# Optimization experiments

Measured on AMD Instinct MI355X. Metric: run time of the kernel, lower is better.

Reference implementation:

```python
import jax, jax.numpy as jnp
import numpy as np

D_MODEL = 1024
N_HEADS = 16
HEAD_DIM = D_MODEL // N_HEADS  # 64
WINDOW = 128
LOCAL_BLOCK = 256
LATENT_TOKENS = 64
LATENT_D = 256
LATENT_HEADS = 4
LATENT_HD = LATENT_D // LATENT_HEADS  # 64
NEG = -1e9


def setup_inputs() -> dict:
    key = jax.random.key(0)
    ks = jax.random.split(key, 14)
    B, S = 2, 4096
    s = 0.02
    f32 = jnp.float32
    return {
        "x": jax.random.normal(ks[0], (B, S, D_MODEL), f32),
        "qkv_w": jax.random.normal(ks[1], (D_MODEL, 3 * D_MODEL), f32) * s,
        "qkv_b": jnp.zeros((3 * D_MODEL,), f32),
        "rq_w": jax.random.normal(ks[2], (D_MODEL, LATENT_D), f32) * s,
        "rq_b": jnp.zeros((LATENT_D,), f32),
        "rkv_w": jax.random.normal(ks[3], (D_MODEL, 2 * LATENT_D), f32) * s,
        "rkv_b": jnp.zeros((2 * LATENT_D,), f32),
        "rout_w": jax.random.normal(ks[4], (LATENT_D, D_MODEL), f32) * s,
        "rout_b": jnp.zeros((D_MODEL,), f32),
        "out_w": jax.random.normal(ks[5], (D_MODEL, D_MODEL), f32) * s,
        "out_b": jnp.zeros((D_MODEL,), f32),
        "gl_w": jax.random.normal(ks[6], (HEAD_DIM, 1), f32) * s,
        "gr_w": jax.random.normal(ks[7], (HEAD_DIM, 1), f32) * s,
    }


def _local_attention(q, k, v):
    # q,k,v: [B,H,S,hd]. Blockwise causal local attention: query i attends to
    # keys at distance d with 0 < d <= WINDOW (strictly past, self excluded).
    B, H, S, hd = q.shape
    bs = min(S, max(WINDOW, LOCAL_BLOCK))
    nb = S // bs  # S chosen divisible by bs
    w = WINDOW
    L = bs + w - 1  # key span per query block
    k_pad = jnp.pad(k, ((0, 0), (0, 0), (w - 1, 0), (0, 0)))
    v_pad = jnp.pad(v, ((0, 0), (0, 0), (w - 1, 0), (0, 0)))
    starts = jnp.arange(nb) * bs
    idx = starts[:, None] + jnp.arange(L)[None, :]  # [nb,L] into padded axis
    kb = k_pad[:, :, idx]  # [B,H,nb,L,hd]
    vb = v_pad[:, :, idx]
    qb = q.reshape(B, H, nb, bs, hd)
    q_pos = starts[:, None] + jnp.arange(bs)[None, :]            # [nb,bs]
    k_gpos = starts[:, None] + jnp.arange(L)[None, :] - (w - 1)   # [nb,L]
    dist = q_pos[:, :, None] - k_gpos[:, None, :]                 # [nb,bs,L]
    allowed = (dist > 0) & (dist <= w) & (k_gpos[:, None, :] >= 0)
    scale = 1.0 / np.sqrt(hd)
    scores = jnp.einsum('bhnqd,bhnkd->bhnqk', qb, kb) * scale
    scores = jnp.where(allowed, scores, NEG)
    attn = jax.nn.softmax(scores, axis=-1)
    # query 0 has no valid keys (self excluded) -> output 0 for that row
    attn = jnp.where(allowed.any(-1)[None, None, :, :, None], attn, 0.0)
    out = jnp.einsum('bhnqk,bhnkd->bhnqd', attn, vb)
    return out.reshape(B, H, S, hd)


def reference(x, qkv_w, qkv_b, rq_w, rq_b, rkv_w, rkv_b, rout_w, rout_b,
              out_w, out_b, gl_w, gr_w):
    B, S, D = x.shape
    # ---- local branch ----
    qkv = x @ qkv_w + qkv_b  # [B,S,3D]
    q, k, v = jnp.split(qkv, 3, axis=-1)
    def heads(t):
        return t.reshape(B, S, N_HEADS, HEAD_DIM).transpose(0, 2, 1, 3)
    local = _local_attention(heads(q), heads(k), heads(v))  # [B,H,S,hd]
    # ---- pooled latents ----
    chunk = -(-S // min(LATENT_TOKENS, S))  # ceil; S divisible here
    nlat = S // chunk
    pooled = x.reshape(B, nlat, chunk, D).mean(axis=2)  # [B,L,D]
    chunk_ids = jnp.arange(S) // chunk                   # [S]
    # ---- latent cross-attention ----
    rq = (x @ rq_w + rq_b).reshape(B, S, LATENT_HEADS, LATENT_HD).transpose(0, 2, 1, 3)
    rkv = pooled @ rkv_w + rkv_b
    rk, rv = jnp.split(rkv, 2, axis=-1)
    rk = rk.reshape(B, nlat, LATENT_HEADS, LATENT_HD).transpose(0, 2, 1, 3)
    rv = rv.reshape(B, nlat, LATENT_HEADS, LATENT_HD).transpose(0, 2, 1, 3)
    lscale = 1.0 / np.sqrt(LATENT_HD)
    lscores = jnp.einsum('bhsd,bhld->bhsl', rq, rk) * lscale  # [B,Hl,S,L]
    lat_allowed = jnp.arange(nlat)[None, :] < chunk_ids[:, None]  # strictly past chunks
    lscores = jnp.where(lat_allowed[None, None], lscores, NEG)
    lattn = jax.nn.softmax(lscores, axis=-1)
    lattn = jnp.where(lat_allowed.any(-1)[None, None, :, None], lattn, 0.0)
    lat_out = jnp.einsum('bhsl,bhld->bhsd', lattn, rv)  # [B,Hl,S,hdl]
    lat_out = lat_out.transpose(0, 2, 1, 3).reshape(B, S, LATENT_D)
    remote = (lat_out @ rout_w + rout_b)                 # [B,S,D]
    remote_h = remote.reshape(B, S, N_HEADS, HEAD_DIM).transpose(0, 2, 1, 3)
    # ---- learned per-head gate mixing local/remote ----
    gate = jax.nn.sigmoid(local @ gl_w + remote_h @ gr_w)  # [B,H,S,1]
    mixed = gate * local + (1.0 - gate) * remote_h
    mixed = mixed.transpose(0, 2, 1, 3).reshape(B, S, D)
    return mixed @ out_w + out_b
```

## Files before the change

### kernel.cpp

```cpp
#include <hip/hip_runtime.h>

typedef __bf16 bf16;
typedef bf16 bf16x4 __attribute__((ext_vector_type(4)));
typedef bf16 bf16x8 __attribute__((ext_vector_type(8)));
typedef float f32x4 __attribute__((ext_vector_type(4)));

#define B_ 2
#define S_ 4096
#define D_ 1024
#define QSTR 3328

__device__ __forceinline__ void gload_lds16(const void* g, void* l) {
  __builtin_amdgcn_global_load_lds((const __attribute__((address_space(1))) void*)g,
                                   (__attribute__((address_space(3))) void*)l, 16, 0, 0);
}

__device__ __forceinline__ void transpose_block(
    const float* __restrict__ in, bf16* __restrict__ out, int K, int N,
    int bx, int by, float (*tile)[33], int tx, int ty)
{
  const int nb = bx * 32, kb = by * 32;
#pragma unroll
  for (int j = 0; j < 4; j++)
    tile[ty + j * 8][tx] = in[(size_t)(kb + ty + j * 8) * N + nb + tx];
  __syncthreads();
#pragma unroll
  for (int j = 0; j < 4; j++)
    out[(size_t)(nb + ty + j * 8) * K + kb + tx] = (bf16)tile[tx][ty + j * 8];
}

__global__ __launch_bounds__(256) void prep_kernel(
    const float* __restrict__ qkv_w, const float* __restrict__ rq_w,
    const float* __restrict__ rkv_w, const float* __restrict__ rout_w,
    const float* __restrict__ out_w, const float* __restrict__ x,
    const float* __restrict__ qkv_b, const float* __restrict__ rq_b,
    bf16* __restrict__ qkvr_wt, bf16* __restrict__ rkv_wt,
    bf16* __restrict__ rout_wt, bf16* __restrict__ out_wt,
    bf16* __restrict__ xb, float* __restrict__ qkvr_b)
{
  __shared__ float tile[32][33];
  const int t = threadIdx.x;
  const int tx = t & 31, ty = t >> 5;
  int bid = blockIdx.x;
  if (bid < 3072) {
    transpose_block(qkv_w, qkvr_wt, 1024, 3072, bid % 96, bid / 96, tile, tx, ty);
    return;
  }
  bid -= 3072;
  if (bid < 256) {
    transpose_block(rq_w, qkvr_wt + (size_t)3072 * 1024, 1024, 256, bid % 8, bid / 8, tile, tx, ty);
    return;
  }
  bid -= 256;
  if (bid < 512) {
    transpose_block(rkv_w, rkv_wt, 1024, 512, bid % 16, bid / 16, tile, tx, ty);
    return;
  }
  bid -= 512;
  if (bid < 256) {
    transpose_block(rout_w, rout_wt, 256, 1024, bid % 32, bid / 32, tile, tx, ty);
    return;
  }
  bid -= 256;
  if (bid < 1024) {
    transpose_block(out_w, out_wt, 1024, 1024, bid % 32, bid / 32, tile, tx, ty);
    return;
  }
  bid -= 1024;
  if (bid < 2048) {
    const int n4 = B_ * S_ * 1024 / 4;
    for (int i = bid * 256 + t; i < n4; i += 2048 * 256) {
      const float4 v = ((const float4*)x)[i];
      bf16x4 o = {(bf16)v.x, (bf16)v.y, (bf16)v.z, (bf16)v.w};
      *(bf16x4*)&xb[i * 4] = o;
    }
    return;
  }
  {
    for (int i = t; i < 3072; i += 256) qkvr_b[i] = qkv_b[i];
    if (t < 256) qkvr_b[3072 + t] = rq_b[t];
  }
}

template <typename OutT>
__global__ __launch_bounds__(256) void gemm_bias_kernel(
    const bf16* __restrict__ A, const bf16* __restrict__ Bt,
    const float* __restrict__ bias, OutT* __restrict__ C,
    int M, int N, int K)
{
  __shared__ __align__(16) bf16 Al[128 * 32];
  __shared__ __align__(16) bf16 Bl[128 * 32];
  const int m0 = blockIdx.x * 128;
  const int n0 = blockIdx.y * 128;
  const int t = threadIdx.x;
  const int lane = t & 63;
  const int wave = t >> 6;
  const int wr = (wave >> 1) * 64;
  const int wc = (wave & 1) * 64;
  const int r16 = lane & 15;
  const int kg = lane >> 4;

  f32x4 acc[4][4];
#pragma unroll
  for (int i = 0; i < 4; i++)
#pragma unroll
    for (int j = 0; j < 4; j++) {
      f32x4 z = {0.f, 0.f, 0.f, 0.f};
      acc[i][j] = z;
    }

  for (int k0 = 0; k0 < K; k0 += 32) {
    __syncthreads();
#pragma unroll
    for (int i = 0; i < 2; i++) {
      const int o = i * 4096 + wave * 1024 + lane * 16;
      const int r = o >> 6;
      const int cb = o & 63;
      gload_lds16((const char*)(A + (size_t)(m0 + r) * K + k0) + cb,
                  (char*)Al + i * 4096 + wave * 1024);
      gload_lds16((const char*)(Bt + (size_t)(n0 + r) * K + k0) + cb,
                  (char*)Bl + i * 4096 + wave * 1024);
    }
    __syncthreads();
    bf16x8 a[4], b[4];
#pragma unroll
    for (int i = 0; i < 4; i++)
      a[i] = *(const bf16x8*)&Al[(wr + i * 16 + r16) * 32 + kg * 8];
#pragma unroll
    for (int i = 0; i < 4; i++)
      b[i] = *(const bf16x8*)&Bl[(wc + i * 16 + r16) * 32 + kg * 8];
#pragma unroll
    for (int i = 0; i < 4; i++)
#pragma unroll
      for (int j = 0; j < 4; j++)
        acc[i][j] = __builtin_amdgcn_mfma_f32_16x16x32_bf16(a[i], b[j], acc[i][j], 0, 0, 0);
  }

  float bs[4];
#pragma unroll
  for (int j = 0; j < 4; j++) bs[j] = bias[n0 + wc + j * 16 + r16];
#pragma unroll
  for (int i = 0; i < 4; i++)
#pragma unroll
    for (int j = 0; j < 4; j++)
#pragma unroll
      for (int r = 0; r < 4; r++) {
        const int row = m0 + wr + i * 16 + kg * 4 + r;
        const int col = n0 + wc + j * 16 + r16;
        C[(size_t)row * N + col] = (OutT)(acc[i][j][r] + bs[j]);
      }
}

template <typename OutT>
__global__ __launch_bounds__(512, 1) void gemm8_kernel(
    const bf16* __restrict__ A, const bf16* __restrict__ Bt,
    const float* __restrict__ bias, OutT* __restrict__ C,
    int M, int N, int K)
{
  __shared__ __align__(16) bf16 Al[2][256 * 64];
  __shared__ __align__(16) bf16 Bl[2][256 * 64];

  const int nbx = gridDim.x;
  const int nwg = nbx * gridDim.y;
  int bid = blockIdx.y * nbx + blockIdx.x;
  bid = (bid & 7) * (nwg >> 3) + (bid >> 3);
  const int m0 = (bid % nbx) * 256;
  const int n0 = (bid / nbx) * 256;

  const int t = threadIdx.x;
  const int lane = t & 63;
  const int w = t >> 6;
  const int wm = w >> 2;
  const int wn = w & 3;
  const int l15 = lane & 15;
  const int kg = lane >> 4;

  const int srow = t >> 3;
  const int schunk = (t & 7) ^ (srow & 7);
  const bf16* Aaddr = A + (size_t)(m0 + srow) * K + schunk * 8;
  const bf16* Baddr = Bt + (size_t)(n0 + srow) * K + schunk * 8;

  const int NT = K >> 6;
  const int NITER = NT >> 1;

  const int arow = wm * 128 + l15;
  const int brow = wn * 64 + l15;
  const int c0 = (kg ^ (l15 & 7)) * 16;
  const int c1 = ((4 + kg) ^ (l15 & 7)) * 16;

  f32x4 acc[8][4];
#pragma unroll
  for (int i = 0; i < 8; i++)
#pragma unroll
    for (int j = 0; j < 4; j++) { f32x4 z = {0, 0, 0, 0}; acc[i][j] = z; }

#define STG_A(buf, q, kt) gload_lds16(Aaddr + (size_t)(q) * 64 * K + (kt) * 64, \
                                      (char*)&Al[buf][0] + (q) * 8192 + w * 1024)
#define STG_B(buf, q, kt) gload_lds16(Baddr + (size_t)(q) * 64 * K + (kt) * 64, \
                                      (char*)&Bl[buf][0] + (q) * 8192 + w * 1024)
#define RD_A(buf, aq) \
  _Pragma("unroll") for (int ii = 0; ii < 4; ii++) { \
    const char* p_ = (const char*)&Al[buf][0] + (size_t)(arow + (aq) * 64 + ii * 16) * 128; \
    af[ii][0] = *(const bf16x8*)(p_ + c0); \
    af[ii][1] = *(const bf16x8*)(p_ + c1); }
#define RD_B(buf) \
  _Pragma("unroll") for (int jj = 0; jj < 4; jj++) { \
    const char* p_ = (const char*)&Bl[buf][0] + (size_t)(brow + jj * 16) * 128; \
    bfr[jj][0] = *(const bf16x8*)(p_ + c0); \
    bfr[jj][1] = *(const bf16x8*)(p_ + c1); }
#define MM(iofs, j0) \
  _Pragma("unroll") for (int ii = 0; ii < 4; ii++) \
  _Pragma("unroll") for (int jj = (j0); jj < (j0) + 2; jj++) { \
    acc[(iofs) + ii][jj] = __builtin_amdgcn_mfma_f32_16x16x32_bf16(af[ii][0], bfr[jj][0], acc[(iofs) + ii][jj], 0, 0, 0); \
    acc[(iofs) + ii][jj] = __builtin_amdgcn_mfma_f32_16x16x32_bf16(af[ii][1], bfr[jj][1], acc[(iofs) + ii][jj], 0, 0, 0); }
#define BARX __builtin_amdgcn_s_barrier()
#define LGKM0 do { asm volatile("s_waitcnt lgkmcnt(0)" ::: "memory"); \
                   __builtin_amdgcn_sched_barrier(0); } while (0)
#define PRI1 __builtin_amdgcn_s_setprio(1)
#define PRI0 __builtin_amdgcn_s_setprio(0)

#pragma unroll
  for (int q = 0; q < 4; q++) { STG_B(0, q, 0); }
#pragma unroll
  for (int q = 0; q < 4; q++) { STG_A(0, q, 0); }
#pragma unroll
  for (int q = 0; q < 4; q++) { STG_B(1, q, 1); }
#pragma unroll
  for (int q = 0; q < 4; q++) { STG_A(1, q, 1); }
  asm volatile("s_waitcnt vmcnt(8)" ::: "memory");
  BARX;

  bf16x8 af[4][2], bfr[4][2];

  for (int it = 0; it < NITER; it++) {
    const int kt0 = 2 * it;
    const bool st = (it + 1) < NITER;

    RD_A(0, 0); RD_B(0);
    BARX; LGKM0; PRI1; MM(0, 0); PRI0; BARX;
    if (st) { STG_B(0, 0, kt0 + 2); STG_B(0, 1, kt0 + 2); }
    PRI1; MM(0, 2); PRI0; BARX;
    RD_A(0, 1);
    if (st) { STG_B(0, 2, kt0 + 2); STG_B(0, 3, kt0 + 2); }
    BARX; LGKM0; PRI1; MM(4, 0); PRI0; BARX;
    if (st) { STG_A(0, 0, kt0 + 2); STG_A(0, 2, kt0 + 2); }
    PRI1; MM(4, 2); PRI0;
    asm volatile("s_waitcnt vmcnt(6)" ::: "memory");
    BARX;

    RD_A(1, 0); RD_B(1);
    if (st) { STG_A(0, 1, kt0 + 2); STG_A(0, 3, kt0 + 2); }
    BARX; LGKM0; PRI1; MM(0, 0); PRI0; BARX;
    if (st) { STG_B(1, 0, kt0 + 3); STG_B(1, 1, kt0 + 3); }
    PRI1; MM(0, 2); PRI0; BARX;
    RD_A(1, 1);
    if (st) { STG_B(1, 2, kt0 + 3); STG_B(1, 3, kt0 + 3); }
    BARX; LGKM0; PRI1; MM(4, 0); PRI0; BARX;
    if (st) { STG_A(1, 0, kt0 + 3); STG_A(1, 1, kt0 + 3);
              STG_A(1, 2, kt0 + 3); STG_A(1, 3, kt0 + 3); }
    PRI1; MM(4, 2); PRI0;
    asm volatile("s_waitcnt vmcnt(8)" ::: "memory");
    BARX;
  }

#undef STG_A
#undef STG_B
#undef RD_A
#undef RD_B
#undef MM
#undef BARX
#undef LGKM0
#undef PRI1
#undef PRI0

  float bs[4];
#pragma unroll
  for (int j = 0; j < 4; j++) bs[j] = bias[n0 + wn * 64 + j * 16 + l15];
#pragma unroll
  for (int i = 0; i < 8; i++)
#pragma unroll
    for (int j = 0; j < 4; j++)
#pragma unroll
      for (int rr = 0; rr < 4; rr++) {
        const int row = m0 + wm * 128 + i * 16 + kg * 4 + rr;
        const int col = n0 + wn * 64 + j * 16 + l15;
        C[(size_t)row * N + col] = (OutT)(acc[i][j][rr] + bs[j]);
      }
}

__global__ __launch_bounds__(256) void pool_rkv_kernel(
    const bf16* __restrict__ xb, const bf16* __restrict__ rkv_wt,
    const float* __restrict__ rkv_b, bf16* __restrict__ rkvb)
{
  __shared__ float prow[1024];
  const int blk = blockIdx.x;
  const int b = blk >> 6, lt = blk & 63;
  const int t = threadIdx.x;

  const bf16* px = xb + ((size_t)b * S_ + lt * 64) * 1024 + t * 4;
  float s0 = 0.f, s1 = 0.f, s2 = 0.f, s3 = 0.f;
#pragma unroll
  for (int c = 0; c < 64; c++) {
    bf16x4 v = *(const bf16x4*)(px + (size_t)c * 1024);
    s0 += (float)v[0]; s1 += (float)v[1]; s2 += (float)v[2]; s3 += (float)v[3];
  }
  prow[t * 4 + 0] = s0 * 0.015625f;
  prow[t * 4 + 1] = s1 * 0.015625f;
  prow[t * 4 + 2] = s2 * 0.015625f;
  prow[t * 4 + 3] = s3 * 0.015625f;
  __syncthreads();

  const int n = blockIdx.y * 256 + t;
  const bf16* wcol = rkv_wt + (size_t)n * 1024;
  float s = rkv_b[n];
#pragma unroll 4
  for (int k = 0; k < 1024; k += 8) {
    bf16x8 wv = *(const bf16x8*)(wcol + k);
#pragma unroll
    for (int j = 0; j < 8; j++) s += prow[k + j] * (float)wv[j];
  }
  rkvb[(size_t)blk * 512 + n] = (bf16)s;
}

__global__ __launch_bounds__(256) void latent_attn_kernel(
    const bf16* __restrict__ qkvrb, const bf16* __restrict__ rkvb,
    bf16* __restrict__ latout)
{
  __shared__ float rq_s[256];
  __shared__ float attn_s[4][64];
  const int blk = blockIdx.x;
  const int b = blk >> 12, s = blk & 4095;
  const int t = threadIdx.x;
  const int h = t >> 6, l = t & 63;
  const int cid = s >> 6;
  rq_s[t] = (float)qkvrb[((size_t)b * S_ + s) * QSTR + 3072 + t];
  __syncthreads();
  float val = -1e30f;
  if (l < cid) {
    const bf16* kr = rkvb + (size_t)(b * 64 + l) * 512 + h * 64;
    float sum = 0.f;
#pragma unroll
    for (int c = 0; c < 8; c++) {
      bf16x8 kv = *(const bf16x8*)(kr + c * 8);
#pragma unroll
      for (int j = 0; j < 8; j++) sum += rq_s[h * 64 + c * 8 + j] * (float)kv[j];
    }
    val = sum * 0.125f;
  }
  float mx = val;
#pragma unroll
  for (int off = 32; off; off >>= 1) mx = fmaxf(mx, __shfl_xor(mx, off));
  const float p = (l < cid) ? __expf(val - mx) : 0.f;
  float sm = p;
#pragma unroll
  for (int off = 32; off; off >>= 1) sm += __shfl_xor(sm, off);
  attn_s[h][l] = (sm > 0.f) ? p / sm : 0.f;
  __syncthreads();
  float o = 0.f;
  const bf16* vb = rkvb + (size_t)b * 64 * 512 + 256 + h * 64 + l;
  for (int lat = 0; lat < cid; lat++) o += attn_s[h][lat] * (float)vb[(size_t)lat * 512];
  latout[((size_t)b * S_ + s) * 256 + h * 64 + l] = (bf16)o;
}

__global__ __launch_bounds__(256) void local_attn_gate(
    const bf16* __restrict__ qkv, const bf16* __restrict__ remote,
    const float* __restrict__ glw, const float* __restrict__ grw,
    bf16* __restrict__ mixedb)
{
  __shared__ __align__(16) bf16 Kl[128 * 72];
  __shared__ __align__(16) bf16 Vt[64 * 136];
  __shared__ __align__(16) bf16 Pl[4][16 * 136];

  const int q0 = blockIdx.x * 128;
  const int h  = blockIdx.y;
  const int b  = blockIdx.z;
  const int t  = threadIdx.x;
  const int w  = t >> 6;
  const int l  = t & 63;
  const int g  = l >> 4;
  const int l15 = l & 15;

  const bf16* qbase = qkv + (size_t)b * S_ * QSTR + h * 64;
  const bf16* kbase = qbase + 1024;
  const bf16* vbase = qbase + 2048;

  bf16* PlW = &Pl[w][0];

  const int kq = (t & 31) * 4;
  const int dh = (t >> 5) * 8;

  bf16x8 qf[2][2];
#pragma unroll
  for (int sl = 0; sl < 2; sl++) {
    const int j = sl ? 7 - w : w;
#pragma unroll
    for (int db = 0; db < 2; db++)
      qf[sl][db] = *(const bf16x8*)(qbase + (size_t)(q0 + j * 16 + l15) * QSTR + db * 32 + g * 8);
  }

  float m_[2][4], l_[2][4];
  f32x4 accO[2][4];
#pragma unroll
  for (int sl = 0; sl < 2; sl++) {
#pragma unroll
    for (int r = 0; r < 4; r++) { m_[sl][r] = -1e30f; l_[sl][r] = 0.f; }
#pragma unroll
    for (int dt = 0; dt < 4; dt++) { f32x4 z = {0,0,0,0}; accO[sl][dt] = z; }
  }

  const int tstart = (q0 == 0) ? 1 : 0;

  bf16x8 kreg[4], vreg[4];
  {
    const int base = q0 - 128 + tstart * 128;
#pragma unroll
    for (int i = 0; i < 4; i++) {
      const int c = i * 256 + t;
      const int kk = c >> 3, dc = c & 7;
      kreg[i] = *(const bf16x8*)(kbase + (size_t)(base + kk) * QSTR + dc * 8);
    }
#pragma unroll
    for (int i = 0; i < 4; i++)
      vreg[i] = *(const bf16x8*)(vbase + (size_t)(base + kq + i) * QSTR + dh);
  }

  for (int tile = tstart; tile < 2; tile++) {
    __syncthreads();
#pragma unroll
    for (int i = 0; i < 4; i++) {
      const int c = i * 256 + t;
      const int kk = c >> 3, dc = c & 7;
      *(bf16x8*)&Kl[kk * 72 + dc * 8] = kreg[i];
    }
#pragma unroll
    for (int j = 0; j < 8; j++) {
      bf16x4 wv = {vreg[0][j], vreg[1][j], vreg[2][j], vreg[3][j]};
      *(bf16x4*)&Vt[(dh + j) * 136 + kq] = wv;
    }
    __syncthreads();
    if (tile == 0) {
#pragma unroll
      for (int i = 0; i < 4; i++) {
        const int c = i * 256 + t;
        const int kk = c >> 3, dc = c & 7;
        kreg[i] = *(const bf16x8*)(kbase + (size_t)(q0 + kk) * QSTR + dc * 8);
      }
#pragma unroll
      for (int i = 0; i < 4; i++)
        vreg[i] = *(const bf16x8*)(vbase + (size_t)(q0 + kq + i) * QSTR + dh);
    }

#pragma unroll
    for (int sl = 0; sl < 2; sl++) {
      const int j = sl ? 7 - w : w;
      const int lo = (tile == 0) ? (j & ~1) : 0;
      const int hi = (tile == 0) ? 8 : ((j & ~1) + 2);

      f32x4 s[8];
#pragma unroll
      for (int kk = 0; kk < 8; kk++) {
        if (kk < lo || kk >= hi) continue;
        f32x4 z = {0,0,0,0};
        s[kk] = z;
        const bf16x8 kf0 = *(const bf16x8*)&Kl[(kk * 16 + l15) * 72 + g * 8];
        const bf16x8 kf1 = *(const bf16x8*)&Kl[(kk * 16 + l15) * 72 + 32 + g * 8];
        s[kk] = __builtin_amdgcn_mfma_f32_16x16x32_bf16(qf[sl][0], kf0, s[kk], 0, 0, 0);
        s[kk] = __builtin_amdgcn_mfma_f32_16x16x32_bf16(qf[sl][1], kf1, s[kk], 0, 0, 0);
      }
#pragma unroll
      for (int kk = 0; kk < 8; kk++) {
        if (kk < lo || kk >= hi) continue;
        const int kr = kk * 16 + l15;
#pragma unroll
        for (int r = 0; r < 4; r++) {
          const int qr = j * 16 + g * 4 + r;
          const bool ok = (tile == 0) ? (kr >= qr) : (kr < qr);
          s[kk][r] = ok ? s[kk][r] * 0.125f : -1e9f;
        }
      }
      float corr[4];
#pragma unroll
      for (int r = 0; r < 4; r++) {
        float v = -1e30f;
#pragma unroll
        for (int kk = 0; kk < 8; kk++) { if (kk < lo || kk >= hi) continue; v = fmaxf(v, s[kk][r]); }
        v = fmaxf(v, __shfl_xor(v, 1));
        v = fmaxf(v, __shfl_xor(v, 2));
        v = fmaxf(v, __shfl_xor(v, 4));
        v = fmaxf(v, __shfl_xor(v, 8));
        const float mn = fmaxf(m_[sl][r], v);
        corr[r] = __expf(m_[sl][r] - mn);
        m_[sl][r] = mn;
      }
      float rs[4] = {0.f, 0.f, 0.f, 0.f};
#pragma unroll
      for (int kk = 0; kk < 8; kk++) {
        if (kk < lo || kk >= hi) continue;
#pragma unroll
        for (int r = 0; r < 4; r++) {
          const float sv = s[kk][r];
          const float p = (sv > -5e8f) ? __expf(sv - m_[sl][r]) : 0.f;
          rs[r] += p;
          PlW[(g * 4 + r) * 136 + kk * 16 + l15] = (bf16)p;
        }
      }
#pragma unroll
      for (int r = 0; r < 4; r++) {
        float v = rs[r];
        v += __shfl_xor(v, 1); v += __shfl_xor(v, 2);
        v += __shfl_xor(v, 4); v += __shfl_xor(v, 8);
        l_[sl][r] = l_[sl][r] * corr[r] + v;
#pragma unroll
        for (int dt = 0; dt < 4; dt++) accO[sl][dt][r] *= corr[r];
      }
      asm volatile("s_waitcnt lgkmcnt(0)" ::: "memory");
      __builtin_amdgcn_sched_barrier(0);
      const int clo = (tile == 0) ? (j >> 1) : 0;
      const int chi = (tile == 0) ? 4 : ((j >> 1) + 1);
#pragma unroll
      for (int kc = 0; kc < 4; kc++) {
        if (kc < clo || kc >= chi) continue;
        const bf16x8 pa = *(const bf16x8*)&PlW[l15 * 136 + kc * 32 + g * 8];
#pragma unroll
        for (int dt = 0; dt < 4; dt++) {
          const bf16x8 vf = *(const bf16x8*)&Vt[(dt * 16 + l15) * 136 + kc * 32 + g * 8];
          accO[sl][dt] = __builtin_amdgcn_mfma_f32_16x16x32_bf16(pa, vf, accO[sl][dt], 0, 0, 0);
        }
      }
    }
  }

  float glv[4], grv[4];
#pragma unroll
  for (int dt = 0; dt < 4; dt++) {
    glv[dt] = glw[dt * 16 + l15];
    grv[dt] = grw[dt * 16 + l15];
  }
  bf16* outp = mixedb + ((size_t)b * S_ + q0) * 1024 + h * 64;
  const bf16* rbase = remote + ((size_t)b * S_ + q0) * 1024 + h * 64;
#pragma unroll
  for (int sl = 0; sl < 2; sl++) {
    const int j = sl ? 7 - w : w;
#pragma unroll
    for (int r = 0; r < 4; r++) {
      const int row = j * 16 + g * 4 + r;
      const float inv = (l_[sl][r] > 0.f) ? 1.f / l_[sl][r] : 0.f;
      float lv[4], rv[4];
      float part = 0.f;
#pragma unroll
      for (int dt = 0; dt < 4; dt++) {
        lv[dt] = accO[sl][dt][r] * inv;
        rv[dt] = (float)rbase[(size_t)row * 1024 + dt * 16 + l15];
        part += lv[dt] * glv[dt] + rv[dt] * grv[dt];
      }
      part += __shfl_xor(part, 1);
      part += __shfl_xor(part, 2);
      part += __shfl_xor(part, 4);
      part += __shfl_xor(part, 8);
      const float gg = 1.f / (1.f + __expf(-part));
#pragma unroll
      for (int dt = 0; dt < 4; dt++)
        outp[(size_t)row * 1024 + dt * 16 + l15] = (bf16)(gg * lv[dt] + (1.f - gg) * rv[dt]);
    }
  }
}

extern "C" void kernel_launch(void* const* d_in, const int* in_sizes, int n_in,
                              void* d_out, int out_size, void* d_ws, size_t ws_size,
                              hipStream_t stream)
{
  const float* x      = (const float*)d_in[0];
  const float* qkv_w  = (const float*)d_in[1];
  const float* qkv_b  = (const float*)d_in[2];
  const float* rq_w   = (const float*)d_in[3];
  const float* rq_b   = (const float*)d_in[4];
  const float* rkv_w  = (const float*)d_in[5];
  const float* rkv_b  = (const float*)d_in[6];
  const float* rout_w = (const float*)d_in[7];
  const float* rout_b = (const float*)d_in[8];
  const float* out_w  = (const float*)d_in[9];
  const float* out_b  = (const float*)d_in[10];
  const float* gl_w   = (const float*)d_in[11];
  const float* gr_w   = (const float*)d_in[12];

  char* w = (char*)d_ws;
  bf16* qkvr_wt = (bf16*)w; w += (size_t)QSTR * 1024 * 2;
  bf16* rkv_wt  = (bf16*)w; w += (size_t)512 * 1024 * 2;
  bf16* rout_wt = (bf16*)w; w += (size_t)1024 * 256 * 2;
  bf16* out_wt  = (bf16*)w; w += (size_t)1024 * 1024 * 2;
  float* qkvr_b = (float*)w; w += (size_t)QSTR * 4;
  bf16* xb      = (bf16*)w; w += (size_t)B_ * S_ * 1024 * 2;
  bf16* qkvrb   = (bf16*)w; w += (size_t)B_ * S_ * QSTR * 2;
  bf16* rkvb    = (bf16*)w; w += (size_t)B_ * 64 * 512 * 2;
  bf16* latout  = (bf16*)w; w += (size_t)B_ * S_ * 256 * 2;
  bf16* remote  = (bf16*)w; w += (size_t)B_ * S_ * 1024 * 2;
  bf16* mixedb  = (bf16*)w; w += (size_t)B_ * S_ * 1024 * 2;

  prep_kernel<<<dim3(7169), 256, 0, stream>>>(qkv_w, rq_w, rkv_w, rout_w, out_w, x,
                                              qkv_b, rq_b,
                                              qkvr_wt, rkv_wt, rout_wt, out_wt, xb, qkvr_b);

  gemm8_kernel<bf16><<<dim3(32, 13), 512, 0, stream>>>(xb, qkvr_wt, qkvr_b, qkvrb, B_ * S_, QSTR, 1024);
  pool_rkv_kernel<<<dim3(128, 2), 256, 0, stream>>>(xb, rkv_wt, rkv_b, rkvb);
  latent_attn_kernel<<<dim3(B_ * S_), 256, 0, stream>>>(qkvrb, rkvb, latout);
  gemm_bias_kernel<bf16><<<dim3(64, 8), 256, 0, stream>>>(latout, rout_wt, rout_b, remote, B_ * S_, 1024, 256);
  local_attn_gate<<<dim3(S_ / 128, 16, B_), 256, 0, stream>>>(qkvrb, remote, gl_w, gr_w, mixedb);
  gemm_bias_kernel<float><<<dim3(64, 8), 256, 0, stream>>>(mixedb, out_wt, out_b, (float*)d_out, B_ * S_, 1024, 1024);
}
```

Baseline: 240.7 us.

## Reorder GEMM LDS waits after MFMA and trade K/V prefetch for occupancy

```diff
diff --git a/kernel.cpp b/kernel.cpp
--- a/kernel.cpp
+++ b/kernel.cpp
@@ -214,8 +214,7 @@
     acc[(iofs) + ii][jj] = __builtin_amdgcn_mfma_f32_16x16x32_bf16(af[ii][0], bfr[jj][0], acc[(iofs) + ii][jj], 0, 0, 0); \
     acc[(iofs) + ii][jj] = __builtin_amdgcn_mfma_f32_16x16x32_bf16(af[ii][1], bfr[jj][1], acc[(iofs) + ii][jj], 0, 0, 0); }
 #define BARX __builtin_amdgcn_s_barrier()
-#define LGKM0 do { asm volatile("s_waitcnt lgkmcnt(0)" ::: "memory"); \
-                   __builtin_amdgcn_sched_barrier(0); } while (0)
+#define LGKMD asm volatile("s_waitcnt lgkmcnt(0)" ::: "memory")
 #define PRI1 __builtin_amdgcn_s_setprio(1)
 #define PRI0 __builtin_amdgcn_s_setprio(0)
 
@@ -237,12 +236,12 @@
     const bool st = (it + 1) < NITER;
 
     RD_A(0, 0); RD_B(0);
-    BARX; LGKM0; PRI1; MM(0, 0); PRI0; BARX;
+    PRI1; MM(0, 0); PRI0; LGKMD; BARX;
     if (st) { STG_B(0, 0, kt0 + 2); STG_B(0, 1, kt0 + 2); }
     PRI1; MM(0, 2); PRI0; BARX;
     RD_A(0, 1);
     if (st) { STG_B(0, 2, kt0 + 2); STG_B(0, 3, kt0 + 2); }
-    BARX; LGKM0; PRI1; MM(4, 0); PRI0; BARX;
+    PRI1; MM(4, 0); PRI0; LGKMD; BARX;
     if (st) { STG_A(0, 0, kt0 + 2); STG_A(0, 2, kt0 + 2); }
     PRI1; MM(4, 2); PRI0;
     asm volatile("s_waitcnt vmcnt(6)" ::: "memory");
@@ -250,12 +249,12 @@
 
     RD_A(1, 0); RD_B(1);
     if (st) { STG_A(0, 1, kt0 + 2); STG_A(0, 3, kt0 + 2); }
-    BARX; LGKM0; PRI1; MM(0, 0); PRI0; BARX;
+    PRI1; MM(0, 0); PRI0; LGKMD; BARX;
     if (st) { STG_B(1, 0, kt0 + 3); STG_B(1, 1, kt0 + 3); }
     PRI1; MM(0, 2); PRI0; BARX;
     RD_A(1, 1);
     if (st) { STG_B(1, 2, kt0 + 3); STG_B(1, 3, kt0 + 3); }
-    BARX; LGKM0; PRI1; MM(4, 0); PRI0; BARX;
+    PRI1; MM(4, 0); PRI0; LGKMD; BARX;
     if (st) { STG_A(1, 0, kt0 + 3); STG_A(1, 1, kt0 + 3);
               STG_A(1, 2, kt0 + 3); STG_A(1, 3, kt0 + 3); }
     PRI1; MM(4, 2); PRI0;
@@ -269,7 +268,7 @@
 #undef RD_B
 #undef MM
 #undef BARX
-#undef LGKM0
+#undef LGKMD
 #undef PRI1
 #undef PRI0
 
@@ -362,7 +361,7 @@
   latout[((size_t)b * S_ + s) * 256 + h * 64 + l] = (bf16)o;
 }
 
-__global__ __launch_bounds__(256) void local_attn_gate(
+__global__ __launch_bounds__(256, 4) void local_attn_gate(
     const bf16* __restrict__ qkv, const bf16* __restrict__ remote,
     const float* __restrict__ glw, const float* __restrict__ grw,
     bf16* __restrict__ mixedb)
@@ -410,9 +409,9 @@
 
   const int tstart = (q0 == 0) ? 1 : 0;
 
-  bf16x8 kreg[4], vreg[4];
-  {
-    const int base = q0 - 128 + tstart * 128;
+  for (int tile = tstart; tile < 2; tile++) {
+    const int base = q0 - 128 + tile * 128;
+    bf16x8 kreg[4], vreg[4];
 #pragma unroll
     for (int i = 0; i < 4; i++) {
       const int c = i * 256 + t;
@@ -422,9 +421,7 @@
 #pragma unroll
     for (int i = 0; i < 4; i++)
       vreg[i] = *(const bf16x8*)(vbase + (size_t)(base + kq + i) * QSTR + dh);
-  }
-
-  for (int tile = tstart; tile < 2; tile++) {
+
     __syncthreads();
 #pragma unroll
     for (int i = 0; i < 4; i++) {
@@ -438,17 +435,6 @@
       *(bf16x4*)&Vt[(dh + j) * 136 + kq] = wv;
     }
     __syncthreads();
-    if (tile == 0) {
-#pragma unroll
-      for (int i = 0; i < 4; i++) {
-        const int c = i * 256 + t;
-        const int kk = c >> 3, dc = c & 7;
-        kreg[i] = *(const bf16x8*)(kbase + (size_t)(q0 + kk) * QSTR + dc * 8);
-      }
-#pragma unroll
-      for (int i = 0; i < 4; i++)
-        vreg[i] = *(const bf16x8*)(vbase + (size_t)(q0 + kq + i) * QSTR + dh);
-    }
 
 #pragma unroll
     for (int sl = 0; sl < 2; sl++) {
```

Measured after the change: 216.5 us. -10.0%, faster.
